# Performance work log

Measured on AMD Instinct MI355X. Metric: run time of the kernel, lower is better.

Reference implementation:

```python
import jax, jax.numpy as jnp
import numpy as np

EMB, HEADS = 1024, 16
HEAD_DIM = EMB // HEADS


def _linear(x, W, b):
    # torch nn.Linear convention: x @ W.T + b, W: [out, in]
    return jnp.einsum('bse,oe->bso', x, W) + b


def setup_inputs() -> dict:
    key = jax.random.key(0)
    ks = jax.random.split(key, 11)
    B, S = 2, 2048
    sc = 1.0 / np.sqrt(EMB)
    inp = {
        'x': jax.random.normal(ks[0], (B, S, EMB), dtype=jnp.float32),
        'y': jax.random.normal(ks[1], (B, S, EMB), dtype=jnp.float32),
        'mask': jnp.ones((B, S, S), dtype=jnp.int32),
        'Wq': jax.random.normal(ks[2], (EMB, EMB), dtype=jnp.float32) * sc,
        'bq': jax.random.normal(ks[3], (EMB,), dtype=jnp.float32) * sc,
        'Wk': jax.random.normal(ks[4], (EMB, EMB), dtype=jnp.float32) * sc,
        'bk': jax.random.normal(ks[5], (EMB,), dtype=jnp.float32) * sc,
        'Wv': jax.random.normal(ks[6], (EMB, EMB), dtype=jnp.float32) * sc,
        'bv': jax.random.normal(ks[7], (EMB,), dtype=jnp.float32) * sc,
        'Wo': jax.random.normal(ks[8], (EMB, EMB), dtype=jnp.float32) * sc,
        'bo': jax.random.normal(ks[9], (EMB,), dtype=jnp.float32) * sc,
    }
    return inp


def reference(x, y, mask, Wq, bq, Wk, bk, Wv, bv, Wo, bo):
    B, S, _ = x.shape
    q = _linear(x, Wq, bq).reshape(B, S, HEADS, HEAD_DIM).transpose(0, 2, 1, 3)
    k = _linear(y, Wk, bk).reshape(B, -1, HEADS, HEAD_DIM).transpose(0, 2, 1, 3)
    v = _linear(y, Wv, bv).reshape(B, -1, HEADS, HEAD_DIM).transpose(0, 2, 1, 3)
    # scores: [B, H, Sq, Sk]
    score = jnp.einsum('bhqd,bhkd->bhqk', q, k) / jnp.sqrt(jnp.float32(HEAD_DIM))
    # NOTE: original torch code calls score.masked_fill(...) without assignment,
    # so the mask has no effect on the computation (faithfully ignored here).
    weights = jax.nn.softmax(score, axis=-1)
    attn = jnp.einsum('bhqk,bhkd->bhqd', weights, v)
    attn = attn.transpose(0, 2, 1, 3).reshape(B, S, EMB)
    # dropout is identity in eval mode
    return _linear(attn, Wo, bo)
```

## Files before the change

kernel.cpp:

```cpp
#include <hip/hip_runtime.h>
#include <cstdint>
#include <cstddef>

#define BB 2
#define SS 2048
#define EE 1024
#define HH 16
#define DD 64

typedef __attribute__((ext_vector_type(8))) short short8;
typedef __attribute__((ext_vector_type(4))) short shortx4;
typedef __attribute__((ext_vector_type(8))) unsigned short ushort8;
typedef __attribute__((ext_vector_type(4))) unsigned short ush4;
typedef __attribute__((ext_vector_type(4))) float floatx4;

#define MFMA32(a, b, c) __builtin_amdgcn_mfma_f32_16x16x32_bf16((a), (b), (c), 0, 0, 0)
#define MFMA16(a, b, c) __builtin_amdgcn_mfma_f32_16x16x16bf16_1k((a), (b), (c), 0, 0, 0)

#define QSCALE 0.18033688011112042f

#define G2L16(g, l)                                                        \
    __builtin_amdgcn_global_load_lds(                                      \
        (const __attribute__((address_space(1))) void*)(g),                \
        (__attribute__((address_space(3))) void*)(l), 16, 0, 0)

__device__ __forceinline__ unsigned short f2bf(float f) {
    unsigned int u = __float_as_uint(f);
    u += 0x7fffu + ((u >> 16) & 1u);
    return (unsigned short)(u >> 16);
}

__device__ __forceinline__ unsigned int pkbf(float a, float b) {
    return __builtin_amdgcn_perm(__float_as_uint(b) + 0x8000u,
                                 __float_as_uint(a) + 0x8000u, 0x07060302u);
}

__global__ __launch_bounds__(256) void k_cvt(
    const float* __restrict__ x, unsigned short* __restrict__ xb,
    const float* __restrict__ y, unsigned short* __restrict__ yb,
    const float* __restrict__ w0, unsigned short* __restrict__ d0,
    const float* __restrict__ w1, unsigned short* __restrict__ d1,
    const float* __restrict__ w2, unsigned short* __restrict__ d2,
    const float* __restrict__ w3, unsigned short* __restrict__ d3)
{
    const int g = blockIdx.y;
    if (g >= 2 && blockIdx.x >= 256) return;
    const float* s = (g == 0) ? x : (g == 1) ? y : (g == 2) ? w0
                   : (g == 3) ? w1 : (g == 4) ? w2 : w3;
    unsigned short* d = (g == 0) ? xb : (g == 1) ? yb : (g == 2) ? d0
                      : (g == 3) ? d1 : (g == 4) ? d2 : d3;
    const size_t i = ((size_t)blockIdx.x * 256 + threadIdx.x) * 16;
    floatx4 f0 = *(const floatx4*)(s + i);
    floatx4 f1 = *(const floatx4*)(s + i + 4);
    floatx4 f2 = *(const floatx4*)(s + i + 8);
    floatx4 f3 = *(const floatx4*)(s + i + 12);
    ushort8 o0, o1;
#pragma unroll
    for (int j = 0; j < 4; ++j) { o0[j] = f2bf(f0[j]); o0[j + 4] = f2bf(f1[j]); }
#pragma unroll
    for (int j = 0; j < 4; ++j) { o1[j] = f2bf(f2[j]); o1[j + 4] = f2bf(f3[j]); }
    *(ushort8*)(d + i) = o0;
    *(ushort8*)(d + i + 8) = o1;
}

template <int MT, int OMODE>
__device__ __forceinline__ void gemm_body(
    const unsigned short* __restrict__ A, const unsigned short* __restrict__ W,
    const float* __restrict__ bias, void* __restrict__ Cv, float oscale,
    int m0, int n0, unsigned short* As0, unsigned short* As1,
    unsigned short* Bs0, unsigned short* Bs1)
{
    constexpr int K = 1024, N = 1024, LDT = 32;
    constexpr int MFR = MT / 32;
    constexpr int KEEP = (MT == 128) ? 4 : 3;
    const int t = threadIdx.x;
    const int lane = t & 63, w = t >> 6;
    const int q = lane >> 4, c = lane & 15;
    const int wm = w & 1, wn = w >> 1;
    const int lr = lane >> 2, lc = (lane & 3) * 8;

    const unsigned short* gA0 = A + (size_t)(m0 + w * (MT / 4) + lr) * K + lc;
    const unsigned short* gA1 = gA0 + 16 * K;
    const unsigned short* gB0 = W + (size_t)(n0 + w * 32 + lr) * K + lc;
    const unsigned short* gB1 = gB0 + 16 * K;
    unsigned short* lA0 = As0 + (w * (MT / 4)) * LDT;
    unsigned short* lA1 = As1 + (w * (MT / 4)) * LDT;
    unsigned short* lB0 = Bs0 + (w * 32) * LDT;
    unsigned short* lB1 = Bs1 + (w * 32) * LDT;

    floatx4 acc[MFR][4] = {};

    auto compute = [&](const unsigned short* Ah, const unsigned short* Bh) {
        short8 af[MFR], bfr[4];
#pragma unroll
        for (int mi = 0; mi < MFR; ++mi)
            af[mi] = *(const short8*)
                &Ah[(wm * (MFR * 16) + mi * 16 + c) * LDT + q * 8];
#pragma unroll
        for (int ni = 0; ni < 4; ++ni)
            bfr[ni] = *(const short8*)
                &Bh[(wn * 64 + ni * 16 + c) * LDT + q * 8];
#pragma unroll
        for (int mi = 0; mi < MFR; ++mi)
#pragma unroll
            for (int ni = 0; ni < 4; ++ni)
                acc[mi][ni] = MFMA32(af[mi], bfr[ni], acc[mi][ni]);
    };

    auto stage = [&](int nk, unsigned short* lA, unsigned short* lB) {
        G2L16(gA0 + nk, lA);
        if constexpr (MT == 128) G2L16(gA1 + nk, lA + 16 * LDT);
        G2L16(gB0 + nk, lB);
        G2L16(gB1 + nk, lB + 16 * LDT);
    };

    stage(0, lA0, lB0);

    for (int kt = 0; kt < K; kt += 64) {
        __builtin_amdgcn_s_barrier();
        stage(kt + 32, lA1, lB1);
        asm volatile("s_waitcnt vmcnt(%0)" :: "n"(KEEP) : "memory");
        __builtin_amdgcn_s_barrier();
        __builtin_amdgcn_sched_barrier(0);
        compute(As0, Bs0);
        __builtin_amdgcn_s_barrier();
        stage((kt + 64) & (K - 1), lA0, lB0);
        asm volatile("s_waitcnt vmcnt(%0)" :: "n"(KEEP) : "memory");
        __builtin_amdgcn_s_barrier();
        __builtin_amdgcn_sched_barrier(0);
        compute(As1, Bs1);
    }

#pragma unroll
    for (int ni = 0; ni < 4; ++ni) {
        const int col = n0 + wn * 64 + ni * 16 + c;
        const float bv = bias[col];
#pragma unroll
        for (int mi = 0; mi < MFR; ++mi)
#pragma unroll
            for (int r = 0; r < 4; ++r) {
                const int row = m0 + wm * (MFR * 16) + mi * 16 + q * 4 + r;
                const float v = (acc[mi][ni][r] + bv) * oscale;
                if constexpr (OMODE == 0) {
                    ((unsigned short*)Cv)[(size_t)row * N + col] = f2bf(v);
                } else if constexpr (OMODE == 1) {
                    const int b = row >> 11, s = row & 2047;
                    ((unsigned short*)Cv)[((size_t)(b * 1024 + col)) * SS + s] = f2bf(v);
                } else {
                    ((float*)Cv)[(size_t)row * N + col] = v;
                }
            }
    }
}

__global__ __launch_bounds__(256) void k_gemm_qkv(
    const unsigned short* __restrict__ x, const unsigned short* __restrict__ y,
    const unsigned short* __restrict__ Wq, const float* __restrict__ bq,
    const unsigned short* __restrict__ Wk, const float* __restrict__ bk,
    const unsigned short* __restrict__ Wv, const float* __restrict__ bv,
    unsigned short* __restrict__ Q, unsigned short* __restrict__ Ko,
    unsigned short* __restrict__ Vt)
{
    __shared__ __align__(16) unsigned short As0[128 * 32], As1[128 * 32];
    __shared__ __align__(16) unsigned short Bs0[128 * 32], Bs1[128 * 32];
    const int m0 = blockIdx.y * 128;
    const int nt = blockIdx.x;
    const int g = nt >> 3;
    const int n0 = (nt & 7) * 128;
    if (g == 0) {
        gemm_body<128, 0>(x, Wq, bq, Q, QSCALE, m0, n0, As0, As1, Bs0, Bs1);
    } else if (g == 1) {
        gemm_body<128, 0>(y, Wk, bk, Ko, 1.0f, m0, n0, As0, As1, Bs0, Bs1);
    } else {
        gemm_body<128, 1>(y, Wv, bv, Vt, 1.0f, m0, n0, As0, As1, Bs0, Bs1);
    }
}

__global__ __launch_bounds__(256) void k_gemm_out(
    const unsigned short* __restrict__ A, const unsigned short* __restrict__ W,
    const float* __restrict__ bias, float* __restrict__ C)
{
    __shared__ __align__(16) unsigned short As0[64 * 32], As1[64 * 32];
    __shared__ __align__(16) unsigned short Bs0[128 * 32], Bs1[128 * 32];
    gemm_body<64, 2>(A, W, bias, C, 1.0f, blockIdx.y * 64, blockIdx.x * 128,
                     As0, As1, Bs0, Bs1);
}

__global__ __launch_bounds__(512, 4) void k_attn(
    const unsigned short* __restrict__ Q, const unsigned short* __restrict__ K,
    const unsigned short* __restrict__ Vt, unsigned short* __restrict__ O)
{
    constexpr int LDK = 72;
    constexpr int TSZ = 64 * LDK + 64 * 64;
    __shared__ __align__(16) unsigned short smem[2 * 2 * TSZ];
    float* Ob = (float*)smem;

    const int bh = blockIdx.x, qt = blockIdx.y;
    const int b = bh >> 4, h = bh & 15;
    const int t = threadIdx.x, w = t >> 6;
    const int ws = w >> 2;
    const int wq = w & 3;
    const int lane = t & 63, q = lane >> 4, c = lane & 15;

    unsigned short* Sb = smem + ws * (2 * TSZ);

    short8 qb[2][2];
#pragma unroll
    for (int g = 0; g < 2; ++g) {
        const size_t qoff =
            (size_t)(b * SS + qt * 128 + wq * 32 + g * 16 + c) * EE + h * DD + q * 8;
        qb[g][0] = *(const short8*)(Q + qoff);
        qb[g][1] = *(const short8*)(Q + qoff + 32);
    }

    floatx4 o[2][4] = {};
    floatx4 lacc[2] = {};
    const shortx4 ones = {(short)0x3F80, (short)0x3F80, (short)0x3F80, (short)0x3F80};

    const int ts = t & 255;
    const int sr = ts >> 2, sp = (ts & 3) * 16;
    const int vkey = (sr & 15) << 2;
    const unsigned short* Kg =
        K + (size_t)(b * SS + ws * 1024 + sr) * EE + h * DD + sp;
    const unsigned short* Vg =
        Vt + ((size_t)bh * DD + sr) * SS + ws * 1024 + sp;

    {
        const ushort8* gk = (const ushort8*)Kg;
        ushort8 k0 = gk[0], k1 = gk[1];
        const ushort8* gv = (const ushort8*)Vg;
        ushort8 v0 = gv[0], v1 = gv[1];
        unsigned short* Ks = Sb;
        unsigned short* Vs = Sb + 64 * LDK;
        *(ushort8*)&Ks[sr * LDK + sp] = k0;
        *(ushort8*)&Ks[sr * LDK + sp + 8] = k1;
        *(ush4*)&Vs[sr * 64 + ((sp +  0) ^ vkey)] =
            __builtin_shufflevector(v0, v0, 0, 1, 2, 3);
        *(ush4*)&Vs[sr * 64 + ((sp +  4) ^ vkey)] =
            __builtin_shufflevector(v0, v0, 4, 5, 6, 7);
        *(ush4*)&Vs[sr * 64 + ((sp +  8) ^ vkey)] =
            __builtin_shufflevector(v1, v1, 0, 1, 2, 3);
        *(ush4*)&Vs[sr * 64 + ((sp + 12) ^ vkey)] =
            __builtin_shufflevector(v1, v1, 4, 5, 6, 7);
    }

#pragma unroll 2
    for (int it = 0; it < 16; ++it) {
        const unsigned short* Ks = Sb + (it & 1) * TSZ;
        const unsigned short* Vs = Ks + 64 * LDK;
        __syncthreads();

        const int nit = (it + 1) & 15;
        ushort8 pk0, pk1, pv0, pv1;
        {
            const ushort8* gk = (const ushort8*)(Kg + (size_t)nit * 64 * EE);
            pk0 = gk[0]; pk1 = gk[1];
            const ushort8* gv = (const ushort8*)(Vg + nit * 64);
            pv0 = gv[0]; pv1 = gv[1];
        }

#pragma unroll
        for (int tt = 0; tt < 4; ++tt) {
            const short8 ka0 = *(const short8*)&Ks[(tt * 16 + c) * LDK + q * 8];
            const short8 ka1 = *(const short8*)&Ks[(tt * 16 + c) * LDK + 32 + q * 8];
            shortx4 pa[2];
#pragma unroll
            for (int g = 0; g < 2; ++g) {
                floatx4 s = {0.f, 0.f, 0.f, 0.f};
                s = MFMA32(ka0, qb[g][0], s);
                s = MFMA32(ka1, qb[g][1], s);
                union { unsigned int u[2]; shortx4 v; } pk;
                pk.u[0] = pkbf(__builtin_amdgcn_exp2f(s[0]),
                               __builtin_amdgcn_exp2f(s[1]));
                pk.u[1] = pkbf(__builtin_amdgcn_exp2f(s[2]),
                               __builtin_amdgcn_exp2f(s[3]));
                pa[g] = pk.v;
            }
#pragma unroll
            for (int nd = 0; nd < 4; ++nd) {
                const shortx4 vb = *(const shortx4*)
                    &Vs[(nd * 16 + c) * 64 + (((tt * 4 + q) ^ c) << 2)];
                o[0][nd] = MFMA16(pa[0], vb, o[0][nd]);
                o[1][nd] = MFMA16(pa[1], vb, o[1][nd]);
            }
            lacc[0] = MFMA16(pa[0], ones, lacc[0]);
            lacc[1] = MFMA16(pa[1], ones, lacc[1]);
        }

        {
            unsigned short* Kn = Sb + ((it + 1) & 1) * TSZ;
            unsigned short* Vn = Kn + 64 * LDK;
            *(ushort8*)&Kn[sr * LDK + sp] = pk0;
            *(ushort8*)&Kn[sr * LDK + sp + 8] = pk1;
            *(ush4*)&Vn[sr * 64 + ((sp +  0) ^ vkey)] =
                __builtin_shufflevector(pv0, pv0, 0, 1, 2, 3);
            *(ush4*)&Vn[sr * 64 + ((sp +  4) ^ vkey)] =
                __builtin_shufflevector(pv0, pv0, 4, 5, 6, 7);
            *(ush4*)&Vn[sr * 64 + ((sp +  8) ^ vkey)] =
                __builtin_shufflevector(pv1, pv1, 0, 1, 2, 3);
            *(ush4*)&Vn[sr * 64 + ((sp + 12) ^ vkey)] =
                __builtin_shufflevector(pv1, pv1, 4, 5, 6, 7);
        }
    }

    __syncthreads();
    if (ws == 1) {
#pragma unroll
        for (int g = 0; g < 2; ++g) {
#pragma unroll
            for (int nd = 0; nd < 4; ++nd)
#pragma unroll
                for (int r = 0; r < 4; ++r)
                    Ob[(wq * 32 + g * 16 + q * 4 + r) * 66 + nd * 16 + c] =
                        o[g][nd][r];
            if (c == 0) {
#pragma unroll
                for (int r = 0; r < 4; ++r)
                    Ob[(wq * 32 + g * 16 + q * 4 + r) * 66 + 64] = lacc[g][r];
            }
        }
    }
    __syncthreads();
    if (ws == 0) {
#pragma unroll
        for (int g = 0; g < 2; ++g) {
            float linv[4];
#pragma unroll
            for (int r = 0; r < 4; ++r) {
                const int rr = wq * 32 + g * 16 + q * 4 + r;
#pragma unroll
                for (int nd = 0; nd < 4; ++nd)
                    o[g][nd][r] += Ob[rr * 66 + nd * 16 + c];
                linv[r] = __builtin_amdgcn_rcpf(lacc[g][r] + Ob[rr * 66 + 64]);
            }
            const int orow = b * SS + qt * 128 + wq * 32 + g * 16;
#pragma unroll
            for (int nd = 0; nd < 4; ++nd)
#pragma unroll
                for (int r = 0; r < 4; ++r)
                    O[(size_t)(orow + q * 4 + r) * EE + h * DD + nd * 16 + c] =
                        f2bf(o[g][nd][r] * linv[r]);
        }
    }
}

extern "C" void kernel_launch(void* const* d_in, const int* in_sizes, int n_in,
                              void* d_out, int out_size, void* d_ws, size_t ws_size,
                              hipStream_t stream)
{
    const float* x  = (const float*)d_in[0];
    const float* y  = (const float*)d_in[1];
    const float* Wq = (const float*)d_in[3];
    const float* bq = (const float*)d_in[4];
    const float* Wk = (const float*)d_in[5];
    const float* bk = (const float*)d_in[6];
    const float* Wv = (const float*)d_in[7];
    const float* bv = (const float*)d_in[8];
    const float* Wo = (const float*)d_in[9];
    const float* bo = (const float*)d_in[10];
    float* out = (float*)d_out;

    char* ws = (char*)d_ws;
    const size_t SZ = (size_t)BB * SS * EE * sizeof(unsigned short);
    const size_t WZ = (size_t)EE * EE * sizeof(unsigned short);
    unsigned short* xb  = (unsigned short*)(ws);
    unsigned short* yb  = (unsigned short*)(ws + SZ);
    unsigned short* Wqb = (unsigned short*)(ws + 2 * SZ);
    unsigned short* Wkb = (unsigned short*)(ws + 2 * SZ + WZ);
    unsigned short* Wvb = (unsigned short*)(ws + 2 * SZ + 2 * WZ);
    unsigned short* Wob = (unsigned short*)(ws + 2 * SZ + 3 * WZ);
    unsigned short* Qw  = (unsigned short*)(ws + 2 * SZ + 4 * WZ);
    unsigned short* Kw  = (unsigned short*)(ws + 3 * SZ + 4 * WZ);
    unsigned short* Vtw = (unsigned short*)(ws + 4 * SZ + 4 * WZ);
    unsigned short* Aw  = (unsigned short*)(ws + 5 * SZ + 4 * WZ);
    (void)ws_size; (void)in_sizes; (void)n_in; (void)out_size;

    k_cvt<<<dim3(1024, 6), 256, 0, stream>>>(x, xb, y, yb, Wq, Wqb, Wk, Wkb,
                                             Wv, Wvb, Wo, Wob);
    k_gemm_qkv<<<dim3(24, 32), 256, 0, stream>>>(xb, yb, Wqb, bq, Wkb, bk, Wvb, bv,
                                                 Qw, Kw, Vtw);
    k_attn<<<dim3(32, 16), 512, 0, stream>>>(Qw, Kw, Vtw, Aw);
    k_gemm_out<<<dim3(8, 64), 256, 0, stream>>>(Aw, Wob, bo, out);
}
```

Measured before the change: 231.6 us.

## Triple-buffer GEMM shared-memory tiles to prefetch two K-steps ahead

Extends the GEMM K-loop from double to triple buffering in LDS, so global-to-LDS loads are issued two stages ahead of compute and the vmcnt wait threshold is raised to match. The loop is restructured into an unrolled three-phase rotation with a tail, and a final vmcnt(0) drains the extra wrapped prefetches. This aims to hide more global memory latency, at the cost of 50% more LDS per block, which may lower occupancy.

```diff
diff --git a/kernel.cpp b/kernel.cpp
--- a/kernel.cpp
+++ b/kernel.cpp
@@ -67,12 +67,13 @@
 __device__ __forceinline__ void gemm_body(
     const unsigned short* __restrict__ A, const unsigned short* __restrict__ W,
     const float* __restrict__ bias, void* __restrict__ Cv, float oscale,
-    int m0, int n0, unsigned short* As0, unsigned short* As1,
-    unsigned short* Bs0, unsigned short* Bs1)
+    int m0, int n0,
+    unsigned short* As0, unsigned short* As1, unsigned short* As2,
+    unsigned short* Bs0, unsigned short* Bs1, unsigned short* Bs2)
 {
     constexpr int K = 1024, N = 1024, LDT = 32;
     constexpr int MFR = MT / 32;
-    constexpr int KEEP = (MT == 128) ? 4 : 3;
+    constexpr int KEEP = (MT == 128) ? 8 : 6;
     const int t = threadIdx.x;
     const int lane = t & 63, w = t >> 6;
     const int q = lane >> 4, c = lane & 15;
@@ -85,8 +86,10 @@
     const unsigned short* gB1 = gB0 + 16 * K;
     unsigned short* lA0 = As0 + (w * (MT / 4)) * LDT;
     unsigned short* lA1 = As1 + (w * (MT / 4)) * LDT;
+    unsigned short* lA2 = As2 + (w * (MT / 4)) * LDT;
     unsigned short* lB0 = Bs0 + (w * 32) * LDT;
     unsigned short* lB1 = Bs1 + (w * 32) * LDT;
+    unsigned short* lB2 = Bs2 + (w * 32) * LDT;
 
     floatx4 acc[MFR][4] = {};
 
@@ -114,22 +117,28 @@
         G2L16(gB1 + nk, lB + 16 * LDT);
     };
 
-    stage(0, lA0, lB0);
-
-    for (int kt = 0; kt < K; kt += 64) {
+    auto phase = [&](int knext, unsigned short* lAn, unsigned short* lBn,
+                     const unsigned short* Ac, const unsigned short* Bc) {
         __builtin_amdgcn_s_barrier();
-        stage(kt + 32, lA1, lB1);
+        stage(knext & (K - 1), lAn, lBn);
         asm volatile("s_waitcnt vmcnt(%0)" :: "n"(KEEP) : "memory");
         __builtin_amdgcn_s_barrier();
         __builtin_amdgcn_sched_barrier(0);
-        compute(As0, Bs0);
-        __builtin_amdgcn_s_barrier();
-        stage((kt + 64) & (K - 1), lA0, lB0);
-        asm volatile("s_waitcnt vmcnt(%0)" :: "n"(KEEP) : "memory");
-        __builtin_amdgcn_s_barrier();
-        __builtin_amdgcn_sched_barrier(0);
-        compute(As1, Bs1);
-    }
+        compute(Ac, Bc);
+    };
+
+    stage(0, lA0, lB0);
+    stage(32, lA1, lB1);
+
+    for (int g = 0; g < 10; ++g) {
+        const int kb = g * 96;
+        phase(kb +  64, lA2, lB2, As0, Bs0);
+        phase(kb +  96, lA0, lB0, As1, Bs1);
+        phase(kb + 128, lA1, lB1, As2, Bs2);
+    }
+    phase(1056, lA2, lB2, As0, Bs0);
+    phase(1088, lA0, lB0, As1, Bs1);
+    asm volatile("s_waitcnt vmcnt(0)" ::: "memory");
 
 #pragma unroll
     for (int ni = 0; ni < 4; ++ni) {
@@ -161,18 +170,23 @@
     unsigned short* __restrict__ Q, unsigned short* __restrict__ Ko,
     unsigned short* __restrict__ Vt)
 {
-    __shared__ __align__(16) unsigned short As0[128 * 32], As1[128 * 32];
-    __shared__ __align__(16) unsigned short Bs0[128 * 32], Bs1[128 * 32];
+    __shared__ __align__(16) unsigned short As0[128 * 32], As1[128 * 32],
+                                            As2[128 * 32];
+    __shared__ __align__(16) unsigned short Bs0[128 * 32], Bs1[128 * 32],
+                                            Bs2[128 * 32];
     const int m0 = blockIdx.y * 128;
     const int nt = blockIdx.x;
     const int g = nt >> 3;
     const int n0 = (nt & 7) * 128;
     if (g == 0) {
-        gemm_body<128, 0>(x, Wq, bq, Q, QSCALE, m0, n0, As0, As1, Bs0, Bs1);
+        gemm_body<128, 0>(x, Wq, bq, Q, QSCALE, m0, n0,
+                          As0, As1, As2, Bs0, Bs1, Bs2);
     } else if (g == 1) {
-        gemm_body<128, 0>(y, Wk, bk, Ko, 1.0f, m0, n0, As0, As1, Bs0, Bs1);
+        gemm_body<128, 0>(y, Wk, bk, Ko, 1.0f, m0, n0,
+                          As0, As1, As2, Bs0, Bs1, Bs2);
     } else {
-        gemm_body<128, 1>(y, Wv, bv, Vt, 1.0f, m0, n0, As0, As1, Bs0, Bs1);
+        gemm_body<128, 1>(y, Wv, bv, Vt, 1.0f, m0, n0,
+                          As0, As1, As2, Bs0, Bs1, Bs2);
     }
 }
 
@@ -180,10 +194,12 @@
     const unsigned short* __restrict__ A, const unsigned short* __restrict__ W,
     const float* __restrict__ bias, float* __restrict__ C)
 {
-    __shared__ __align__(16) unsigned short As0[64 * 32], As1[64 * 32];
-    __shared__ __align__(16) unsigned short Bs0[128 * 32], Bs1[128 * 32];
+    __shared__ __align__(16) unsigned short As0[64 * 32], As1[64 * 32],
+                                            As2[64 * 32];
+    __shared__ __align__(16) unsigned short Bs0[128 * 32], Bs1[128 * 32],
+                                            Bs2[128 * 32];
     gemm_body<64, 2>(A, W, bias, C, 1.0f, blockIdx.y * 64, blockIdx.x * 128,
-                     As0, As1, Bs0, Bs1);
+                     As0, As1, As2, Bs0, Bs1, Bs2);
 }
 
 __global__ __launch_bounds__(512, 4) void k_attn(
```

After: 226.1 us. -2.4%, faster.
